# Performance work log

Measured on AMD Instinct MI355X. Metric: run time of the kernel, lower is better.

Reference implementation:

```python
import jax, jax.numpy as jnp
import numpy as np

# model geometry (matches init_kwargs cfg)
D = 768        # D_EMB
PATCH = 16
T = 8192
N = T // PATCH # 512 patch tokens
H = 12         # heads
HD = D // H    # 64 head dim
NL = 6         # layers
DFF = 4 * D
B = 8
LN_EPS = 1e-5


def setup_inputs() -> dict:
    key = jax.random.key(0)
    ks = iter(jax.random.split(key, 32))
    def g(shape, scale=0.02):
        return jax.random.normal(next(ks), shape, jnp.float32) * scale
    return dict(
        x=jax.random.normal(next(ks), (B, T), jnp.float32),
        pp_w=g((D, PATCH)), pp_b=jnp.zeros((D,), jnp.float32),
        pe=g((N, D)),
        ln1_g=jnp.ones((NL, D), jnp.float32), ln1_b=jnp.zeros((NL, D), jnp.float32),
        qkv_w=g((NL, 3 * D, D)), out_w=g((NL, D, D)),
        ln2_g=jnp.ones((NL, D), jnp.float32), ln2_b=jnp.zeros((NL, D), jnp.float32),
        fc1_w=g((NL, DFF, D)), fc2_w=g((NL, D, DFF)),
        lnf_g=jnp.ones((D,), jnp.float32), lnf_b=jnp.zeros((D,), jnp.float32),
        h1_w=g((D // 2, D)), h1_b=jnp.zeros((D // 2,), jnp.float32),
        h2_w=g((2, D // 2)), h2_b=jnp.zeros((2,), jnp.float32),
    )


def _ln(x, g, b):
    m = x.mean(-1, keepdims=True)
    v = ((x - m) ** 2).mean(-1, keepdims=True)
    return (x - m) / jnp.sqrt(v + LN_EPS) * g + b


def reference(x, pp_w, pp_b, pe, ln1_g, ln1_b, qkv_w, out_w,
              ln2_g, ln2_b, fc1_w, fc2_w, lnf_g, lnf_b,
              h1_w, h1_b, h2_w, h2_b):
    Bx = x.shape[0]
    # patch embed: [B, N, PATCH] @ W^T + b -> [B, N, D]
    z = jnp.einsum('bnp,dp->bnd', x[:, :N * PATCH].reshape(Bx, N, PATCH), pp_w) + pp_b
    z = z + pe  # positional embedding (arange indexes whole table)
    mask = jnp.tril(jnp.ones((N, N), dtype=bool))
    for i in range(NL):
        # --- attention (manual causal softmax, dropout=eval/no-op) ---
        h = _ln(z, ln1_g[i], ln1_b[i])
        qkv = jnp.einsum('bnd,ed->bne', h, qkv_w[i])            # [B,N,3D]
        qkv = qkv.reshape(Bx, N, 3, H, HD).transpose(2, 0, 3, 1, 4)
        q, k, v = qkv[0], qkv[1], qkv[2]                         # [B,H,N,HD]
        s = jnp.einsum('bhld,bhmd->bhlm', q, k) / np.sqrt(HD)
        s = jnp.where(mask, s, -jnp.inf)
        a = jax.nn.softmax(s, axis=-1)
        o = jnp.einsum('bhlm,bhmd->bhld', a, v)
        o = o.transpose(0, 2, 1, 3).reshape(Bx, N, D)
        z = z + jnp.einsum('bnd,ed->bne', o, out_w[i])
        # --- FFN (exact gelu, matching F.gelu default) ---
        h = _ln(z, ln2_g[i], ln2_b[i])
        f = jax.nn.gelu(jnp.einsum('bnd,fd->bnf', h, fc1_w[i]), approximate=False)
        z = z + jnp.einsum('bnf,df->bnd', f, fc2_w[i])
    enc = _ln(z, lnf_g, lnf_b).mean(axis=1)                      # [B, D]
    y = jax.nn.relu(enc @ h1_w.T + h1_b)
    return y @ h2_w.T + h2_b                                     # [B, 2]
```

## Files before the change

kernel.cpp:

```cpp
#include <hip/hip_runtime.h>
#include <hip/hip_bf16.h>
#include <math.h>

#define D_EMB 768
#define NPATCH 16
#define NTOK 512
#define NHEAD 12
#define HDIM 64
#define NLAYER 6
#define DFF 3072
#define BATCH 8
#define MTOK (BATCH * NTOK)

typedef __attribute__((ext_vector_type(8))) short bf16x8;
typedef __attribute__((ext_vector_type(4))) float f32x4;

__device__ __forceinline__ float bf2f(ushort s) {
    unsigned u = ((unsigned)s) << 16;
    return __builtin_bit_cast(float, u);
}
__device__ __forceinline__ ushort f2bf(float f) {
    unsigned u = __builtin_bit_cast(unsigned, f);
    unsigned r = (u + 0x7FFFu + ((u >> 16) & 1u)) >> 16;
    return (ushort)r;
}

__global__ __launch_bounds__(256)
void f2bf4_kernel(const float* __restrict__ s0, ushort* __restrict__ d0, int n0,
                  const float* __restrict__ s1, ushort* __restrict__ d1, int n1,
                  const float* __restrict__ s2, ushort* __restrict__ d2, int n2,
                  const float* __restrict__ s3, ushort* __restrict__ d3, int n3)
{
    int i = blockIdx.x * 256 + threadIdx.x;
    const float* s; ushort* d; int off;
    if (i < n0)                { s = s0; d = d0; off = i; }
    else if (i < n0 + n1)      { s = s1; d = d1; off = i - n0; }
    else if (i < n0 + n1 + n2) { s = s2; d = d2; off = i - n0 - n1; }
    else if (i < n0 + n1 + n2 + n3) { s = s3; d = d3; off = i - n0 - n1 - n2; }
    else return;
    float4 v = *(const float4*)(s + (size_t)off * 4);
    ushort4 o;
    o.x = f2bf(v.x); o.y = f2bf(v.y); o.z = f2bf(v.z); o.w = f2bf(v.w);
    *(ushort4*)(d + (size_t)off * 4) = o;
}

__global__ __launch_bounds__(256)
void patch_embed_kernel(const float* __restrict__ x, const float* __restrict__ pw,
                        const float* __restrict__ pb, const float* __restrict__ pe,
                        float* __restrict__ z)
{
    int bn = blockIdx.x;
    int b = bn >> 9, n = bn & 511;
    __shared__ float xs[NPATCH];
    int t = threadIdx.x;
    if (t < NPATCH) xs[t] = x[(size_t)b * 8192 + n * NPATCH + t];
    __syncthreads();
    for (int d = t; d < D_EMB; d += 256) {
        float acc = pb[d] + pe[(size_t)n * D_EMB + d];
        const float* w = pw + (size_t)d * NPATCH;
        #pragma unroll
        for (int p = 0; p < NPATCH; ++p) acc += xs[p] * w[p];
        z[(size_t)bn * D_EMB + d] = acc;
    }
}

__device__ __forceinline__ float block_reduce_sum_256(float v)
{
    __shared__ float lds[4];
    #pragma unroll
    for (int o = 32; o > 0; o >>= 1) v += __shfl_xor(v, o);
    int lane = threadIdx.x & 63, wid = threadIdx.x >> 6;
    __syncthreads();
    if (lane == 0) lds[wid] = v;
    __syncthreads();
    return lds[0] + lds[1] + lds[2] + lds[3];
}

__device__ __forceinline__ void store_val(float* p, float v)  { *p = v; }
__device__ __forceinline__ void store_val(ushort* p, float v) { *p = f2bf(v); }

template<typename OT>
__global__ __launch_bounds__(256)
void ln_kernel(const float* __restrict__ x, const float* __restrict__ g,
               const float* __restrict__ bta, OT* __restrict__ y)
{
    int row = blockIdx.x;
    const float* xr = x + (size_t)row * D_EMB;
    int t = threadIdx.x;
    float vals[3];
    float s = 0.f;
    #pragma unroll
    for (int i = 0; i < 3; ++i) { vals[i] = xr[t + i * 256]; s += vals[i]; }
    float mean = block_reduce_sum_256(s) * (1.0f / D_EMB);
    float ss = 0.f;
    #pragma unroll
    for (int i = 0; i < 3; ++i) { float d = vals[i] - mean; ss += d * d; }
    float var = block_reduce_sum_256(ss) * (1.0f / D_EMB);
    float rstd = rsqrtf(var + 1e-5f);
    #pragma unroll
    for (int i = 0; i < 3; ++i) {
        int d = t + i * 256;
        store_val(y + (size_t)row * D_EMB + d, (vals[i] - mean) * rstd * g[d] + bta[d]);
    }
}

#define STAGE64(buf, k0)                                                           \
    {                                                                              \
        _Pragma("unroll")                                                          \
        for (int j = 0; j < 2; ++j) {                                              \
            int row = j * 32 + srow;                                               \
            int lcol = pcol ^ (row & 7);                                           \
            const ushort* sa = Ab + (size_t)(bm + row) * lda + (k0) + (lcol << 3); \
            __builtin_amdgcn_global_load_lds(                                      \
                (const __attribute__((address_space(1))) unsigned int*)sa,         \
                (__attribute__((address_space(3))) unsigned int*)&As[buf][row * 64 + (pcol << 3)], \
                16, 0, 0);                                                         \
        }                                                                          \
        _Pragma("unroll")                                                          \
        for (int j = 0; j < 4; ++j) {                                              \
            int row = j * 32 + srow;                                               \
            int lcol = pcol ^ (row & 7);                                           \
            const ushort* sb = Wb + (size_t)(bn + row) * lda + (k0) + (lcol << 3); \
            __builtin_amdgcn_global_load_lds(                                      \
                (const __attribute__((address_space(1))) unsigned int*)sb,         \
                (__attribute__((address_space(3))) unsigned int*)&Bs[buf][row * 64 + (pcol << 3)], \
                16, 0, 0);                                                         \
        }                                                                          \
    }

#define COMPUTE64(buf)                                                             \
    {                                                                              \
        _Pragma("unroll")                                                          \
        for (int kk = 0; kk < 64; kk += 32) {                                      \
            int c = (kk >> 3) + lg;                                                \
            bf16x8 a[4], b[2];                                                     \
            _Pragma("unroll")                                                      \
            for (int m = 0; m < 4; ++m) {                                          \
                int row = m * 16 + lr;                                             \
                a[m] = *(const bf16x8*)(&As[buf][row * 64 + ((c ^ (row & 7)) << 3)]); \
            }                                                                      \
            _Pragma("unroll")                                                      \
            for (int n = 0; n < 2; ++n) {                                          \
                int row = w * 32 + n * 16 + lr;                                    \
                b[n] = *(const bf16x8*)(&Bs[buf][row * 64 + ((c ^ (row & 7)) << 3)]); \
            }                                                                      \
            _Pragma("unroll")                                                      \
            for (int m = 0; m < 4; ++m) {                                          \
                _Pragma("unroll")                                                  \
                for (int n = 0; n < 2; ++n)                                        \
                    acc[m][n] = __builtin_amdgcn_mfma_f32_16x16x32_bf16(a[m], b[n], acc[m][n], 0, 0, 0); \
            }                                                                      \
        }                                                                          \
    }

template<int EPI, typename OT, bool SPLITK>
__global__ __launch_bounds__(256)
void mfma_gemm(const ushort* __restrict__ A,
               const ushort* __restrict__ W,
               OT* __restrict__ C,
               const float* __restrict__ res,
               int N, int K, int lda)
{
    __shared__ ushort As[2][64 * 64];
    __shared__ ushort Bs[2][128 * 64];

    int gx = gridDim.x, gy = gridDim.y;
    int bx = blockIdx.x, by = blockIdx.y;
    int bz = SPLITK ? blockIdx.z : 0;
    if ((gy & 7) == 0) {
        int flat = bx + gx * (by + gy * bz);
        int xcd = flat & 7, j = flat >> 3;
        int ry = gy >> 3;
        by = xcd * ry + (j % ry);
        int rem = j / ry;
        bx = rem % gx;
        bz = rem / gx;
    }
    int bm = by * 64, bn = bx * 128;

    const ushort* Ab = A + (size_t)bz * K;
    const ushort* Wb = W + (size_t)bz * K;
    OT* Cb = C + (SPLITK ? (size_t)bz * ((size_t)gy * 64) * N : 0);

    int tid = threadIdx.x;
    int w = tid >> 6, l = tid & 63;
    int lr = l & 15, lg = l >> 4;
    f32x4 acc[4][2] = {};

    int srow = w * 8 + (l >> 3);
    int pcol = l & 7;

    const int nk = K >> 6;
    STAGE64(0, 0);
    __syncthreads();
    int cur = 0;
    for (int t = 0; t < nk; ++t) {
        if (t + 1 < nk) STAGE64(cur ^ 1, (t + 1) << 6);
        COMPUTE64(cur);
        __syncthreads();
        cur ^= 1;
    }

    int r0 = lg * 4;
    #pragma unroll
    for (int m = 0; m < 4; ++m) {
        #pragma unroll
        for (int n = 0; n < 2; ++n) {
            #pragma unroll
            for (int j = 0; j < 4; ++j) {
                int gm = bm + m * 16 + r0 + j;
                int gn = bn + w * 32 + n * 16 + lr;
                float v = acc[m][n][j];
                if (EPI == 1) v = 0.5f * v * (1.0f + erff(v * 0.70710678118654752f));
                if (EPI == 2) v += res[(size_t)gm * N + gn];
                store_val(Cb + (size_t)gm * N + gn, v);
            }
        }
    }
}

__global__ __launch_bounds__(256)
void splitk_reduce(const float* __restrict__ p, float* __restrict__ z, int n4)
{
    int i = blockIdx.x * 256 + threadIdx.x;
    if (i >= n4) return;
    float4 a = ((const float4*)p)[i];
    float4 b = ((const float4*)p)[i + (size_t)n4];
    float4 c = ((float4*)z)[i];
    c.x += a.x + b.x; c.y += a.y + b.y; c.z += a.z + b.z; c.w += a.w + b.w;
    ((float4*)z)[i] = c;
}

__global__ __launch_bounds__(256)
void attn_mfma_kernel(const ushort* __restrict__ qkv, ushort* __restrict__ o)
{
    int w = threadIdx.x >> 6, l = threadIdx.x & 63;
    int qt = blockIdx.x * 4 + w;
    int h = blockIdx.y, b = blockIdx.z;
    int q0 = qt * 16;
    int lr = l & 15, lg = l >> 4;

    const size_t rs = 3 * D_EMB;
    const ushort* qbase = qkv + ((size_t)(b * NTOK)) * rs + h * HDIM;
    const ushort* kbase = qbase + D_EMB;
    const ushort* vbase = qbase + 2 * D_EMB;

    bf16x8 qf[2];
    qf[0] = *(const bf16x8*)(qbase + (size_t)(q0 + lr) * rs + lg * 8);
    qf[1] = *(const bf16x8*)(qbase + (size_t)(q0 + lr) * rs + 32 + lg * 8);

    f32x4 oacc[4] = {};
    float m_j[4], l_j[4];
    #pragma unroll
    for (int j = 0; j < 4; ++j) { m_j[j] = -1e30f; l_j[j] = 0.f; }

    __shared__ ushort P_lds[4][16][40];

    int ntiles = q0 / 32 + 1;
    for (int mt = 0; mt < ntiles; ++mt) {
        int m0 = mt * 32;
        f32x4 s[2] = {};
        #pragma unroll
        for (int kb = 0; kb < 2; ++kb) {
            const ushort* kr = kbase + (size_t)(m0 + kb * 16 + lr) * rs;
            bf16x8 k0 = *(const bf16x8*)(kr + lg * 8);
            bf16x8 k1 = *(const bf16x8*)(kr + 32 + lg * 8);
            s[kb] = __builtin_amdgcn_mfma_f32_16x16x32_bf16(qf[0], k0, s[kb], 0, 0, 0);
            s[kb] = __builtin_amdgcn_mfma_f32_16x16x32_bf16(qf[1], k1, s[kb], 0, 0, 0);
        }
        bool partial = (m0 + 31 > q0);
        float p[2][4], mx[4];
        #pragma unroll
        for (int j = 0; j < 4; ++j) {
            int qr = q0 + lg * 4 + j;
            float s0 = s[0][j] * 0.125f;
            float s1 = s[1][j] * 0.125f;
            if (partial) {
                if (m0 + lr > qr)      s0 = -1e30f;
                if (m0 + 16 + lr > qr) s1 = -1e30f;
            }
            p[0][j] = s0; p[1][j] = s1;
            float mm = fmaxf(s0, s1);
            mm = fmaxf(mm, __shfl_xor(mm, 1));
            mm = fmaxf(mm, __shfl_xor(mm, 2));
            mm = fmaxf(mm, __shfl_xor(mm, 4));
            mm = fmaxf(mm, __shfl_xor(mm, 8));
            mx[j] = mm;
        }
        #pragma unroll
        for (int j = 0; j < 4; ++j) {
            float mnew = fmaxf(m_j[j], mx[j]);
            float scale = __expf(m_j[j] - mnew);
            float p0 = __expf(p[0][j] - mnew);
            float p1 = __expf(p[1][j] - mnew);
            p[0][j] = p0; p[1][j] = p1;
            float rsum = p0 + p1;
            rsum += __shfl_xor(rsum, 1);
            rsum += __shfl_xor(rsum, 2);
            rsum += __shfl_xor(rsum, 4);
            rsum += __shfl_xor(rsum, 8);
            l_j[j] = l_j[j] * scale + rsum;
            m_j[j] = mnew;
            #pragma unroll
            for (int i = 0; i < 4; ++i) oacc[i][j] *= scale;
        }
        #pragma unroll
        for (int kb = 0; kb < 2; ++kb)
            #pragma unroll
            for (int j = 0; j < 4; ++j)
                P_lds[w][lg * 4 + j][kb * 16 + lr] = f2bf(p[kb][j]);
        asm volatile("s_waitcnt lgkmcnt(0)" ::: "memory");
        bf16x8 pa = *(const bf16x8*)(&P_lds[w][lr][lg * 8]);
        #pragma unroll
        for (int i = 0; i < 4; ++i) {
            bf16x8 vf;
            const ushort* vp = vbase + (size_t)(m0 + lg * 8) * rs + i * 16 + lr;
            #pragma unroll
            for (int j = 0; j < 8; ++j) vf[j] = (short)vp[(size_t)j * rs];
            oacc[i] = __builtin_amdgcn_mfma_f32_16x16x32_bf16(pa, vf, oacc[i], 0, 0, 0);
        }
    }
    #pragma unroll
    for (int i = 0; i < 4; ++i) {
        #pragma unroll
        for (int j = 0; j < 4; ++j) {
            int qr = q0 + lg * 4 + j;
            int d  = i * 16 + lr;
            float v = oacc[i][j] / l_j[j];
            o[((size_t)(b * NTOK + qr)) * D_EMB + h * HDIM + d] = f2bf(v);
        }
    }
}

__global__ void mean_kernel(const float* __restrict__ x, float* __restrict__ enc)
{
    int b = blockIdx.x; int d = threadIdx.x;
    float s = 0.f;
    for (int n = 0; n < NTOK; ++n) s += x[((size_t)(b * NTOK + n)) * D_EMB + d];
    enc[b * D_EMB + d] = s * (1.0f / NTOK);
}

__global__ void head1_kernel(const float* __restrict__ enc, const float* __restrict__ w,
                             const float* __restrict__ bias, float* __restrict__ r)
{
    int b = blockIdx.x; int j = threadIdx.x;
    float acc = bias[j];
    const float* e = enc + b * D_EMB;
    const float* wr = w + (size_t)j * D_EMB;
    for (int k = 0; k < D_EMB; ++k) acc += e[k] * wr[k];
    r[b * 384 + j] = fmaxf(acc, 0.f);
}

__global__ void head2_kernel(const float* __restrict__ r, const float* __restrict__ w,
                             const float* __restrict__ bias, float* __restrict__ out)
{
    int idx = threadIdx.x;
    if (idx >= 16) return;
    int b = idx >> 1, j = idx & 1;
    float acc = bias[j];
    for (int k = 0; k < 384; ++k) acc += r[b * 384 + k] * w[j * 384 + k];
    out[b * 2 + j] = acc;
}

extern "C" void kernel_launch(void* const* d_in, const int* in_sizes, int n_in,
                              void* d_out, int out_size, void* d_ws, size_t ws_size,
                              hipStream_t stream)
{
    const float* x     = (const float*)d_in[0];
    const float* pp_w  = (const float*)d_in[1];
    const float* pp_b  = (const float*)d_in[2];
    const float* pe    = (const float*)d_in[3];
    const float* ln1_g = (const float*)d_in[4];
    const float* ln1_b = (const float*)d_in[5];
    const float* qkv_w = (const float*)d_in[6];
    const float* out_w = (const float*)d_in[7];
    const float* ln2_g = (const float*)d_in[8];
    const float* ln2_b = (const float*)d_in[9];
    const float* fc1_w = (const float*)d_in[10];
    const float* fc2_w = (const float*)d_in[11];
    const float* lnf_g = (const float*)d_in[12];
    const float* lnf_b = (const float*)d_in[13];
    const float* h1_w  = (const float*)d_in[14];
    const float* h1_b  = (const float*)d_in[15];
    const float* h2_w  = (const float*)d_in[16];
    const float* h2_b  = (const float*)d_in[17];
    float* out = (float*)d_out;

    char* p = (char*)d_ws;
    float*  z      = (float*)p;  p += (size_t)MTOK * D_EMB * 4;
    ushort* big_bf = (ushort*)p; p += (size_t)MTOK * DFF * 2;
    ushort* h_bf   = (ushort*)p; p += (size_t)MTOK * D_EMB * 2;
    ushort* wq_bf  = (ushort*)p; p += (size_t)3 * D_EMB * D_EMB * 2;
    ushort* wo_bf  = (ushort*)p; p += (size_t)D_EMB * D_EMB * 2;
    ushort* wf1_bf = (ushort*)p; p += (size_t)DFF * D_EMB * 2;
    ushort* wf2_bf = (ushort*)p; p += (size_t)D_EMB * DFF * 2;
    float*  pbuf   = (float*)p;  p += (size_t)2 * MTOK * D_EMB * 4;
    float*  enc    = (float*)p;  p += BATCH * D_EMB * 4;
    float*  r1     = (float*)p;  p += BATCH * 384 * 4;
    float*  lnf_out = (float*)big_bf;

    patch_embed_kernel<<<MTOK, 256, 0, stream>>>(x, pp_w, pp_b, pe, z);

    const int nq = 3 * D_EMB * D_EMB, no = D_EMB * D_EMB, nf = DFF * D_EMB;
    const int n4q = nq / 4, n4o = no / 4, n4f = nf / 4;
    const int cvt_blocks = (n4q + n4o + 2 * n4f + 255) / 256;
    const int n4red = MTOK * D_EMB / 4;

    for (int i = 0; i < NLAYER; ++i) {
        f2bf4_kernel<<<cvt_blocks, 256, 0, stream>>>(
            qkv_w + (size_t)i * nq, wq_bf,  n4q,
            out_w + (size_t)i * no, wo_bf,  n4o,
            fc1_w + (size_t)i * nf, wf1_bf, n4f,
            fc2_w + (size_t)i * nf, wf2_bf, n4f);

        ln_kernel<ushort><<<MTOK, 256, 0, stream>>>(z, ln1_g + i * D_EMB, ln1_b + i * D_EMB, h_bf);

        dim3 gq((3 * D_EMB) / 128, MTOK / 64);
        mfma_gemm<0, ushort, false><<<gq, 256, 0, stream>>>(h_bf, wq_bf, big_bf, nullptr,
                                                            3 * D_EMB, D_EMB, D_EMB);

        dim3 ga(NTOK / 64, NHEAD, BATCH);
        attn_mfma_kernel<<<ga, 256, 0, stream>>>(big_bf, h_bf);

        dim3 gp(D_EMB / 128, MTOK / 64);
        mfma_gemm<2, float, false><<<gp, 256, 0, stream>>>(h_bf, wo_bf, z, z,
                                                           D_EMB, D_EMB, D_EMB);

        ln_kernel<ushort><<<MTOK, 256, 0, stream>>>(z, ln2_g + i * D_EMB, ln2_b + i * D_EMB, h_bf);

        dim3 g1(DFF / 128, MTOK / 64);
        mfma_gemm<1, ushort, false><<<g1, 256, 0, stream>>>(h_bf, wf1_bf, big_bf, nullptr,
                                                            DFF, D_EMB, D_EMB);

        dim3 g2(D_EMB / 128, MTOK / 64, 2);
        mfma_gemm<0, float, true><<<g2, 256, 0, stream>>>(big_bf, wf2_bf, pbuf, nullptr,
                                                          D_EMB, DFF / 2, DFF);
        splitk_reduce<<<(n4red + 255) / 256, 256, 0, stream>>>(pbuf, z, n4red);
    }

    ln_kernel<float><<<MTOK, 256, 0, stream>>>(z, lnf_g, lnf_b, lnf_out);
    mean_kernel<<<BATCH, D_EMB, 0, stream>>>(lnf_out, enc);
    head1_kernel<<<BATCH, 384, 0, stream>>>(enc, h1_w, h1_b, r1);
    head2_kernel<<<1, 64, 0, stream>>>(r1, h2_w, h2_b, out);
}
```

Measured before the change: 1.110 ms.

## Fuse split-K reduce with next LayerNorm and widen QKV/FC1 GEMM tiles

The split-K partial-sum reduction is merged into the following LayerNorm (the next layer's ln1, or the final LN), so the residual update and normalization happen in one pass instead of two separate kernels. A new GEMM variant with 64x256 tiles (each wave computing 64 columns) is used for the QKV and FC1 projections to increase data reuse per LDS load. The wider tile doubles B-tile shared memory to 64 KB total and raises accumulator registers, which may reduce occupancy and cuts the grid to half the blocks.

Measured after the change: 1.195 ms. 1.08x slower.

```diff
diff --git a/kernel.cpp b/kernel.cpp
--- a/kernel.cpp
+++ b/kernel.cpp
@@ -103,6 +103,41 @@
         store_val(y + (size_t)row * D_EMB + d, (vals[i] - mean) * rstd * g[d] + bta[d]);
     }
 }
+
+template<typename OT>
+__global__ __launch_bounds__(256)
+void reduce_ln_kernel(const float* __restrict__ pbuf, float* __restrict__ z,
+                      const float* __restrict__ g, const float* __restrict__ bta,
+                      OT* __restrict__ y)
+{
+    int row = blockIdx.x;
+    int t = threadIdx.x;
+    const float* p0 = pbuf + (size_t)row * D_EMB;
+    const float* p1 = pbuf + (size_t)MTOK * D_EMB + (size_t)row * D_EMB;
+    float* zr = z + (size_t)row * D_EMB;
+    float vals[3];
+    float s = 0.f;
+    #pragma unroll
+    for (int i = 0; i < 3; ++i) {
+        int d = t + i * 256;
+        float v = zr[d] + p0[d] + p1[d];
+        vals[i] = v;
+        zr[d] = v;
+        s += v;
+    }
+    float mean = block_reduce_sum_256(s) * (1.0f / D_EMB);
+    float ss = 0.f;
+    #pragma unroll
+    for (int i = 0; i < 3; ++i) { float d = vals[i] - mean; ss += d * d; }
+    float var = block_reduce_sum_256(ss) * (1.0f / D_EMB);
+    float rstd = rsqrtf(var + 1e-5f);
+    #pragma unroll
+    for (int i = 0; i < 3; ++i) {
+        int d = t + i * 256;
+        store_val(y + (size_t)row * D_EMB + d, (vals[i] - mean) * rstd * g[d] + bta[d]);
+    }
+}
+
 
 #define STAGE64(buf, k0)                                                           \
     {                                                                              \
@@ -131,8 +166,8 @@
 #define COMPUTE64(buf)                                                             \
     {                                                                              \
         _Pragma("unroll")                                                          \
-        for (int kk = 0; kk < 64; kk += 32) {                                      \
-            int c = (kk >> 3) + lg;                                                \
+        for (int kk = 0; kk < 2; ++kk) {                                           \
+            int c = kk * 4 + lg;                                                   \
             bf16x8 a[4], b[2];                                                     \
             _Pragma("unroll")                                                      \
             for (int m = 0; m < 4; ++m) {                                          \
@@ -155,10 +190,8 @@
 
 template<int EPI, typename OT, bool SPLITK>
 __global__ __launch_bounds__(256)
-void mfma_gemm(const ushort* __restrict__ A,
-               const ushort* __restrict__ W,
-               OT* __restrict__ C,
-               const float* __restrict__ res,
+void mfma_gemm(const ushort* __restrict__ A, const ushort* __restrict__ W,
+               OT* __restrict__ C, const float* __restrict__ res,
                int N, int K, int lda)
 {
     __shared__ ushort As[2][64 * 64];
@@ -219,16 +252,111 @@
     }
 }
 
-__global__ __launch_bounds__(256)
-void splitk_reduce(const float* __restrict__ p, float* __restrict__ z, int n4)
-{
-    int i = blockIdx.x * 256 + threadIdx.x;
-    if (i >= n4) return;
-    float4 a = ((const float4*)p)[i];
-    float4 b = ((const float4*)p)[i + (size_t)n4];
-    float4 c = ((float4*)z)[i];
-    c.x += a.x + b.x; c.y += a.y + b.y; c.z += a.z + b.z; c.w += a.w + b.w;
-    ((float4*)z)[i] = c;
+#define STAGEW(buf, k0)                                                            \
+    {                                                                              \
+        _Pragma("unroll")                                                          \
+        for (int j = 0; j < 2; ++j) {                                              \
+            int row = j * 32 + srow;                                               \
+            int lcol = pcol ^ (row & 7);                                           \
+            const ushort* sa = Ab + (size_t)(bm + row) * lda + (k0) + (lcol << 3); \
+            __builtin_amdgcn_global_load_lds(                                      \
+                (const __attribute__((address_space(1))) unsigned int*)sa,         \
+                (__attribute__((address_space(3))) unsigned int*)&As[buf][row * 64 + (pcol << 3)], \
+                16, 0, 0);                                                         \
+        }                                                                          \
+        _Pragma("unroll")                                                          \
+        for (int j = 0; j < 8; ++j) {                                              \
+            int row = j * 32 + srow;                                               \
+            int lcol = pcol ^ (row & 7);                                           \
+            const ushort* sb = Wb + (size_t)(bn + row) * lda + (k0) + (lcol << 3); \
+            __builtin_amdgcn_global_load_lds(                                      \
+                (const __attribute__((address_space(1))) unsigned int*)sb,         \
+                (__attribute__((address_space(3))) unsigned int*)&Bs[buf][row * 64 + (pcol << 3)], \
+                16, 0, 0);                                                         \
+        }                                                                          \
+    }
+
+#define COMPUTEW(buf)                                                              \
+    {                                                                              \
+        _Pragma("unroll")                                                          \
+        for (int kk = 0; kk < 2; ++kk) {                                           \
+            int c = kk * 4 + lg;                                                   \
+            bf16x8 a[4], b[4];                                                     \
+            _Pragma("unroll")                                                      \
+            for (int m = 0; m < 4; ++m) {                                          \
+                int row = m * 16 + lr;                                             \
+                a[m] = *(const bf16x8*)(&As[buf][row * 64 + ((c ^ (row & 7)) << 3)]); \
+            }                                                                      \
+            _Pragma("unroll")                                                      \
+            for (int n = 0; n < 4; ++n) {                                          \
+                int row = w * 64 + n * 16 + lr;                                    \
+                b[n] = *(const bf16x8*)(&Bs[buf][row * 64 + ((c ^ (row & 7)) << 3)]); \
+            }                                                                      \
+            _Pragma("unroll")                                                      \
+            for (int m = 0; m < 4; ++m) {                                          \
+                _Pragma("unroll")                                                  \
+                for (int n = 0; n < 4; ++n)                                        \
+                    acc[m][n] = __builtin_amdgcn_mfma_f32_16x16x32_bf16(a[m], b[n], acc[m][n], 0, 0, 0); \
+            }                                                                      \
+        }                                                                          \
+    }
+
+template<int EPI, typename OT>
+__global__ __launch_bounds__(256)
+void mfma_gemm_w(const ushort* __restrict__ A, const ushort* __restrict__ W,
+                 OT* __restrict__ C, int N, int K, int lda)
+{
+    __shared__ ushort As[2][64 * 64];
+    __shared__ ushort Bs[2][256 * 64];
+
+    int gx = gridDim.x, gy = gridDim.y;
+    int bx = blockIdx.x, by = blockIdx.y;
+    if ((gy & 7) == 0) {
+        int flat = bx + gx * by;
+        int xcd = flat & 7, j = flat >> 3;
+        int ry = gy >> 3;
+        by = xcd * ry + (j % ry);
+        bx = (j / ry) % gx;
+    }
+    int bm = by * 64, bn = bx * 256;
+
+    const ushort* Ab = A;
+    const ushort* Wb = W;
+
+    int tid = threadIdx.x;
+    int w = tid >> 6, l = tid & 63;
+    int lr = l & 15, lg = l >> 4;
+    f32x4 acc[4][4] = {};
+
+    int srow = w * 8 + (l >> 3);
+    int pcol = l & 7;
+
+    const int nk = K >> 6;
+    STAGEW(0, 0);
+    __syncthreads();
+    int cur = 0;
+    for (int t = 0; t < nk; ++t) {
+        if (t + 1 < nk) STAGEW(cur ^ 1, (t + 1) << 6);
+        COMPUTEW(cur);
+        __syncthreads();
+        cur ^= 1;
+    }
+
+    int r0 = lg * 4;
+    #pragma unroll
+    for (int m = 0; m < 4; ++m) {
+        #pragma unroll
+        for (int n = 0; n < 4; ++n) {
+            #pragma unroll
+            for (int j = 0; j < 4; ++j) {
+                int gm = bm + m * 16 + r0 + j;
+                int gn = bn + w * 64 + n * 16 + lr;
+                float v = acc[m][n][j];
+                if (EPI == 1) v = 0.5f * v * (1.0f + erff(v * 0.70710678118654752f));
+                store_val(C + (size_t)gm * N + gn, v);
+            }
+        }
+    }
 }
 
 __global__ __launch_bounds__(256)
@@ -404,7 +532,8 @@
     const int nq = 3 * D_EMB * D_EMB, no = D_EMB * D_EMB, nf = DFF * D_EMB;
     const int n4q = nq / 4, n4o = no / 4, n4f = nf / 4;
     const int cvt_blocks = (n4q + n4o + 2 * n4f + 255) / 256;
-    const int n4red = MTOK * D_EMB / 4;
+
+    ln_kernel<ushort><<<MTOK, 256, 0, stream>>>(z, ln1_g, ln1_b, h_bf);
 
     for (int i = 0; i < NLAYER; ++i) {
         f2bf4_kernel<<<cvt_blocks, 256, 0, stream>>>(
@@ -413,11 +542,9 @@
             fc1_w + (size_t)i * nf, wf1_bf, n4f,
             fc2_w + (size_t)i * nf, wf2_bf, n4f);
 
-        ln_kernel<ushort><<<MTOK, 256, 0, stream>>>(z, ln1_g + i * D_EMB, ln1_b + i * D_EMB, h_bf);
-
-        dim3 gq((3 * D_EMB) / 128, MTOK / 64);
-        mfma_gemm<0, ushort, false><<<gq, 256, 0, stream>>>(h_bf, wq_bf, big_bf, nullptr,
-                                                            3 * D_EMB, D_EMB, D_EMB);
+        dim3 gq((3 * D_EMB) / 256, MTOK / 64);
+        mfma_gemm_w<0, ushort><<<gq, 256, 0, stream>>>(h_bf, wq_bf, big_bf,
+                                                       3 * D_EMB, D_EMB, D_EMB);
 
         dim3 ga(NTOK / 64, NHEAD, BATCH);
         attn_mfma_kernel<<<ga, 256, 0, stream>>>(big_bf, h_bf);
@@ -428,17 +555,23 @@
 
         ln_kernel<ushort><<<MTOK, 256, 0, stream>>>(z, ln2_g + i * D_EMB, ln2_b + i * D_EMB, h_bf);
 
-        dim3 g1(DFF / 128, MTOK / 64);
-        mfma_gemm<1, ushort, false><<<g1, 256, 0, stream>>>(h_bf, wf1_bf, big_bf, nullptr,
-                                                            DFF, D_EMB, D_EMB);
+        dim3 g1(DFF / 256, MTOK / 64);
+        mfma_gemm_w<1, ushort><<<g1, 256, 0, stream>>>(h_bf, wf1_bf, big_bf,
+                                                       DFF, D_EMB, D_EMB);
 
         dim3 g2(D_EMB / 128, MTOK / 64, 2);
         mfma_gemm<0, float, true><<<g2, 256, 0, stream>>>(big_bf, wf2_bf, pbuf, nullptr,
                                                           D_EMB, DFF / 2, DFF);
-        splitk_reduce<<<(n4red + 255) / 256, 256, 0, stream>>>(pbuf, z, n4red);
-    }
-
-    ln_kernel<float><<<MTOK, 256, 0, stream>>>(z, lnf_g, lnf_b, lnf_out);
+
+        if (i < NLAYER - 1) {
+            reduce_ln_kernel<ushort><<<MTOK, 256, 0, stream>>>(
+                pbuf, z, ln1_g + (i + 1) * D_EMB, ln1_b + (i + 1) * D_EMB, h_bf);
+        } else {
+            reduce_ln_kernel<float><<<MTOK, 256, 0, stream>>>(
+                pbuf, z, lnf_g, lnf_b, lnf_out);
+        }
+    }
+
     mean_kernel<<<BATCH, D_EMB, 0, stream>>>(lnf_out, enc);
     head1_kernel<<<BATCH, 384, 0, stream>>>(enc, h1_w, h1_b, r1);
     head2_kernel<<<1, 64, 0, stream>>>(r1, h2_w, h2_b, out);
```
